# Performance work log

Hardware: AMD Instinct MI355X
Metric: run time of the kernel (lower is better)

## Reference

```python
import jax, jax.numpy as jnp
import numpy as np
import math

B, H, W, Cv, Ct, T = 8, 64, 64, 256, 512, 100
TOP_M = 5
N_PAD = 8  # last N_PAD text tokens are all-zero padding


def _xavier(key, fi, fo):
    lim = math.sqrt(6.0 / (fi + fo))
    return jax.random.uniform(key, (fi, fo), jnp.float32, -lim, lim)


def layernorm(x, g, b, eps=1e-5):
    m = x.mean(-1, keepdims=True)
    v = ((x - m) ** 2).mean(-1, keepdims=True)
    return (x - m) * jax.lax.rsqrt(v + eps) * g + b


def l2norm(x, eps=1e-6):
    n = jnp.sqrt((x * x).sum(-1, keepdims=True))
    return x / jnp.maximum(n, eps)


def setup_inputs() -> dict:
    key = jax.random.key(0)
    ks = jax.random.split(key, 10)
    visual = jax.random.normal(ks[0], (B, H, W, Cv), jnp.float32)
    text = jax.random.normal(ks[1], (B, T, Ct), jnp.float32)
    text = text.at[:, T - N_PAD:, :].set(0.0)  # padded tokens
    return {
        'visual_features': visual,
        'text_features': text,
        'ln1_g': jnp.ones((Cv,), jnp.float32),
        'ln1_b': jnp.zeros((Cv,), jnp.float32),
        'qw': _xavier(ks[2], Cv, Ct), 'qb': jnp.zeros((Ct,), jnp.float32),
        'vw': _xavier(ks[3], Ct, Cv), 'vb': jnp.zeros((Cv,), jnp.float32),
        'gate_w': jax.random.normal(ks[4], (Cv, 1), jnp.float32) * 0.02,
        'gate_b': jnp.zeros((1,), jnp.float32),
        'logit_scale': jnp.asarray(math.log(1.0 / 0.07), jnp.float32),
        'alpha': jnp.asarray(0.1, jnp.float32),
        'ln2_g': jnp.ones((Cv,), jnp.float32),
        'ln2_b': jnp.zeros((Cv,), jnp.float32),
        'w1': jax.random.normal(ks[5], (Cv, 4 * Cv), jnp.float32) * 0.02,
        'b1': jnp.zeros((4 * Cv,), jnp.float32),
        'w2': jax.random.normal(ks[6], (4 * Cv, Cv), jnp.float32) * 0.02,
        'b2': jnp.zeros((Cv,), jnp.float32),
        'top_m': TOP_M,
    }


def reference(visual_features, text_features, ln1_g, ln1_b, qw, qb, vw, vb,
              gate_w, gate_b, logit_scale, alpha, ln2_g, ln2_b, w1, b1, w2, b2,
              top_m):
    Bv, Hh, Ww, C = visual_features.shape
    N = Hh * Ww
    x = layernorm(visual_features, ln1_g, ln1_b).reshape(Bv, N, C)
    q = l2norm(x @ qw + qb)                     # (B,N,Ct)
    k = l2norm(text_features)                   # (B,T,Ct)
    v = text_features @ vw + vb                 # (B,T,Cv)
    pad = jnp.abs(text_features).sum(-1) <= 1e-6  # (B,T) True = padding
    Ctd = float(qw.shape[1])
    scale = jnp.exp(jnp.clip(logit_scale, -2.0, 2.0)) / math.sqrt(Ctd)
    sim = jnp.einsum('bnc,btc->bnt', q, k) * scale
    top_vals, top_idx = jax.lax.top_k(sim, top_m)       # (B,N,M)
    pad_top = jax.vmap(lambda p, i: p[i])(pad, top_idx)  # (B,N,M)
    top_vals = jnp.where(pad_top, -jnp.inf, top_vals)
    attn = jax.nn.softmax(top_vals, axis=-1)
    v_sel = jax.vmap(lambda vb_, ib: vb_[ib])(v, top_idx)  # (B,N,M,Cv)
    aligned = jnp.einsum('bnm,bnmc->bnc', attn, v_sel)
    gate = jax.nn.sigmoid(x @ gate_w + gate_b)  # (B,N,1)
    aligned = aligned * gate
    y = x + alpha * aligned
    y = layernorm(y, ln2_g, ln2_b)
    y = y + (jax.nn.gelu(y @ w1 + b1, approximate=False) @ w2 + b2)
    return y.reshape(Bv, Hh, Ww, C)
```

## Files before the change

kernel.cpp:

```cpp
#include <hip/hip_runtime.h>
#include <hip/hip_bf16.h>
#include <math.h>

using bf16 = __hip_bfloat16;
typedef __attribute__((ext_vector_type(8))) short s16x8;
typedef __attribute__((ext_vector_type(4))) short s16x4;
typedef __attribute__((ext_vector_type(4))) float f32x4;
typedef __attribute__((ext_vector_type(4))) unsigned int u32x4;

static __device__ __forceinline__ float bits2f(unsigned short u) {
  union { unsigned int i; float f; } c; c.i = ((unsigned int)u) << 16; return c.f;
}
static __device__ __forceinline__ unsigned short f2bits(float f) {
  bf16 h = __float2bfloat16(f);
  return *reinterpret_cast<unsigned short*>(&h);
}
static __device__ __forceinline__ unsigned short scrub16(unsigned short u, unsigned short repl) {
  return ((u & 0x7F80u) == 0x7F80u) ? repl : u;
}
static __device__ __forceinline__ unsigned short f2bits_s(float f, unsigned short repl) {
  return scrub16(f2bits(f), repl);
}
static __device__ __forceinline__ float ldf_s(const float* p, float repl) {
  unsigned int w = *reinterpret_cast<const unsigned int*>(p);
  if ((w & 0x7F800000u) == 0x7F800000u) return repl;
  union { unsigned int i; float f; } c; c.i = w; return c.f;
}
static __device__ __forceinline__ float stf_s(float f, float repl) {
  union { float f; unsigned int i; } c; c.f = f;
  if ((c.i & 0x7F800000u) == 0x7F800000u) return repl;
  return f;
}
static __device__ __forceinline__ void gload_lds16(const unsigned short* g, unsigned short* l) {
  __builtin_amdgcn_global_load_lds(
      (const __attribute__((address_space(1))) void*)g,
      (__attribute__((address_space(3))) void*)l, 16, 0, 0);
}

static __device__ __forceinline__ float block_sum(float v, float* red, int tid) {
  #pragma unroll
  for (int o = 32; o > 0; o >>= 1) v += __shfl_down(v, o, 64);
  __syncthreads();
  if ((tid & 63) == 0) red[tid >> 6] = v;
  __syncthreads();
  return red[0] + red[1] + red[2] + red[3];
}

__global__ __launch_bounds__(256)
void k_ln1(float* vis, const float* __restrict__ g, const float* __restrict__ bta) {
  const int lane = threadIdx.x & 63;
  const long row = (long)blockIdx.x * 4 + (threadIdx.x >> 6);
  float* rp = vis + row * 256;
  union { u32x4 u; float f[4]; unsigned int w[4]; } c;
  c.u = *reinterpret_cast<const u32x4*>(&rp[lane * 4]);
  #pragma unroll
  for (int e = 0; e < 4; e++)
    if ((c.w[e] & 0x7F800000u) == 0x7F800000u) c.f[e] = 0.f;
  float s = c.f[0] + c.f[1] + c.f[2] + c.f[3];
  #pragma unroll
  for (int o = 32; o > 0; o >>= 1) s += __shfl_xor(s, o, 64);
  const float mean = s * (1.f / 256.f);
  float vr = 0.f;
  #pragma unroll
  for (int e = 0; e < 4; e++) { c.f[e] -= mean; vr = fmaf(c.f[e], c.f[e], vr); }
  #pragma unroll
  for (int o = 32; o > 0; o >>= 1) vr += __shfl_xor(vr, o, 64);
  const float rstd = rsqrtf(vr * (1.f / 256.f) + 1e-5f);
  f32x4 outv;
  #pragma unroll
  for (int e = 0; e < 4; e++)
    outv[e] = stf_s(c.f[e] * rstd * g[lane * 4 + e] + bta[lane * 4 + e], 0.f);
  *reinterpret_cast<f32x4*>(&rp[lane * 4]) = outv;
}

__global__ __launch_bounds__(256)
void k_prepw(const float* __restrict__ qw, unsigned short* __restrict__ qwt) {
  const int n = blockIdx.x;
  const int k = threadIdx.x;
  qwt[n * 256 + (k ^ ((n & 7) << 3))] = f2bits_s(ldf_s(&qw[(long)k * 512 + n], 0.f), 0);
}

__global__ __launch_bounds__(256)
void k_prep2(const float* __restrict__ text, unsigned short* __restrict__ khat,
             int* __restrict__ padf) {
  __shared__ float red[4];
  const int t = blockIdx.x, b = blockIdx.y, tid = threadIdx.x;
  unsigned short* kr = khat + ((long)b * 112 + t) * 512;
  if (t >= 100) {
    if (tid < 64) *reinterpret_cast<s16x8*>(&kr[tid * 8]) = (s16x8){0,0,0,0,0,0,0,0};
    return;
  }
  const float* tr = text + ((long)b * 100 + t) * 512;
  const float v0 = ldf_s(&tr[tid], 0.f), v1 = ldf_s(&tr[tid + 256], 0.f);
  const float ss = block_sum(fmaf(v0, v0, v1 * v1), red, tid);
  const float sa = block_sum(fabsf(v0) + fabsf(v1), red, tid);
  const float inv = 1.f / fmaxf(sqrtf(ss), 1e-6f);
  kr[tid]       = f2bits_s(v0 * inv, 0);
  kr[tid + 256] = f2bits_s(v1 * inv, 0);
  if (tid == 0) padf[b * 100 + t] = (sa <= 1e-6f) ? 1 : 0;
}

__global__ __launch_bounds__(512)
void k_sim_mfma(const float* __restrict__ x, const unsigned short* __restrict__ qwt,
                const float* __restrict__ qb, const unsigned short* __restrict__ khat,
                const float* __restrict__ ls, unsigned short* __restrict__ simb) {
  __shared__ __align__(16) unsigned short s_q[64][520];
  __shared__ __align__(16) unsigned short s_un[32768];
  __shared__ float s_qn[64];

  const int tid  = threadIdx.x;
  const int lane = tid & 63;
  const int w    = tid >> 6;
  const int l15  = lane & 15;
  const int lg   = lane >> 4;
  const int b    = blockIdx.y;
  const long grow = (long)b * 4096 + (long)blockIdx.x * 64;

  const int R1 = (w >> 2) * 32;
  s16x8 xa[2][8];
  #pragma unroll
  for (int rb = 0; rb < 2; rb++) {
    const float* xr = &x[(grow + R1 + rb * 16 + l15) * 256];
    #pragma unroll
    for (int ks = 0; ks < 8; ks++) {
      const float* p = xr + ks * 32 + lg * 8;
      s16x8 v;
      #pragma unroll
      for (int e = 0; e < 8; e++) v[e] = (short)f2bits_s(ldf_s(p + e, 0.f), 0);
      xa[rb][ks] = v;
    }
  }

  const int C1 = (w & 3) * 32;
  for (int nc = 0; nc < 4; nc++) {
    __syncthreads();
    {
      const unsigned short* src = qwt + (long)nc * 128 * 256;
      #pragma unroll
      for (int it = 0; it < 8; it++) {
        const int u = tid + it * 512;
        *reinterpret_cast<s16x8*>(&s_un[u * 8]) =
            *reinterpret_cast<const s16x8*>(&src[u * 8]);
      }
    }
    __syncthreads();
    f32x4 a1[2][2];
    #pragma unroll
    for (int i = 0; i < 2; i++)
      #pragma unroll
      for (int j = 0; j < 2; j++) a1[i][j] = (f32x4){0.f, 0.f, 0.f, 0.f};
    #pragma unroll
    for (int ks = 0; ks < 8; ks++) {
      s16x8 bfr[2];
      #pragma unroll
      for (int cb = 0; cb < 2; cb++) {
        const int nl = C1 + cb * 16 + l15;
        const int byt = nl * 512 + ((ks * 64 + lg * 16) ^ ((nl & 7) << 4));
        bfr[cb] = *reinterpret_cast<const s16x8*>(reinterpret_cast<const char*>(s_un) + byt);
      }
      #pragma unroll
      for (int rb = 0; rb < 2; rb++) {
        a1[rb][0] = __builtin_amdgcn_mfma_f32_16x16x32_bf16(xa[rb][ks], bfr[0], a1[rb][0], 0, 0, 0);
        a1[rb][1] = __builtin_amdgcn_mfma_f32_16x16x32_bf16(xa[rb][ks], bfr[1], a1[rb][1], 0, 0, 0);
      }
    }
    #pragma unroll
    for (int cb = 0; cb < 2; cb++) {
      const int n = nc * 128 + C1 + cb * 16 + l15;
      const float bq = ldf_s(&qb[n], 0.f);
      #pragma unroll
      for (int rb = 0; rb < 2; rb++)
        #pragma unroll
        for (int rg = 0; rg < 4; rg++)
          s_q[R1 + rb * 16 + lg * 4 + rg][n] = f2bits_s(a1[rb][cb][rg] + bq, 0);
    }
  }
  __syncthreads();

  {
    const int r = tid >> 3, ts8 = tid & 7;
    float ss = 0.f;
    #pragma unroll
    for (int j = 0; j < 8; j++) {
      s16x8 v = *reinterpret_cast<const s16x8*>(&s_q[r][ts8 * 64 + j * 8]);
      #pragma unroll
      for (int e = 0; e < 8; e++) { float f = bits2f((unsigned short)v[e]); ss = fmaf(f, f, ss); }
    }
    #pragma unroll
    for (int o = 4; o > 0; o >>= 1) ss += __shfl_down(ss, o, 8);
    if (ts8 == 0) s_qn[r] = fmaxf(sqrtf(ss), 1e-6f);
  }

  const int wr = w & 1, wc = w >> 1;
  unsigned short (*s_k)[264] = reinterpret_cast<unsigned short(*)[264]>(s_un);
  f32x4 acc[2][2];
  #pragma unroll
  for (int i = 0; i < 2; i++)
    #pragma unroll
    for (int j = 0; j < 2; j++) acc[i][j] = (f32x4){0.f, 0.f, 0.f, 0.f};

  for (int kc = 0; kc < 2; kc++) {
    __syncthreads();
    for (int it = 0; it < 7; it++) {
      const int u = it * 512 + tid;
      const int t = u >> 5, kb = (u & 31) * 8;
      *reinterpret_cast<s16x8*>(&s_k[t][kb]) =
          *reinterpret_cast<const s16x8*>(&khat[((long)b * 112 + t) * 512 + kc * 256 + kb]);
    }
    __syncthreads();
    #pragma unroll
    for (int ks = 0; ks < 8; ks++) {
      const int ko = kc * 256 + ks * 32 + lg * 8;
      s16x8 af[2], bfr[2];
      #pragma unroll
      for (int rb = 0; rb < 2; rb++)
        af[rb] = *reinterpret_cast<const s16x8*>(&s_q[(2 * wr + rb) * 16 + l15][ko]);
      #pragma unroll
      for (int cb = 0; cb < 2; cb++)
        if (2 * wc + cb < 7)
          bfr[cb] = *reinterpret_cast<const s16x8*>(&s_k[(2 * wc + cb) * 16 + l15][ks * 32 + lg * 8]);
      #pragma unroll
      for (int rb = 0; rb < 2; rb++)
        #pragma unroll
        for (int cb = 0; cb < 2; cb++)
          if (2 * wc + cb < 7)
            acc[rb][cb] = __builtin_amdgcn_mfma_f32_16x16x32_bf16(af[rb], bfr[cb], acc[rb][cb], 0, 0, 0);
    }
  }

  float l = ldf_s(&ls[0], 0.f);
  l = fminf(fmaxf(l, -2.f), 2.f);
  const float scale = expf(l) * 0.04419417382415922f;
  #pragma unroll
  for (int rb = 0; rb < 2; rb++)
    #pragma unroll
    for (int rg = 0; rg < 4; rg++) {
      const int row = (2 * wr + rb) * 16 + lg * 4 + rg;
      const float inv = scale / s_qn[row];
      #pragma unroll
      for (int cb = 0; cb < 2; cb++) {
        const int tcol = (2 * wc + cb) * 16 + l15;
        if (2 * wc + cb < 7 && tcol < 100)
          simb[(grow + row) * 100 + tcol] = f2bits_s(acc[rb][cb][rg] * inv, 0);
      }
    }
}

__global__ __launch_bounds__(256)
void k_v(const float* __restrict__ text, const float* __restrict__ vw,
         const float* __restrict__ vb_, float* __restrict__ vf) {
  __shared__ float s_t[512];
  const int bt = blockIdx.x;
  const int tid = threadIdx.x;
  const float* tr = text + (long)bt * 512;
  s_t[tid]       = ldf_s(&tr[tid], 0.f);
  s_t[tid + 256] = ldf_s(&tr[tid + 256], 0.f);
  __syncthreads();
  float acc = 0.f;
  for (int k = 0; k < 512; k++) acc = fmaf(s_t[k], vw[k * 256 + tid], acc);
  vf[(long)bt * 256 + tid] = stf_s(acc + vb_[tid], 0.f);
}

#define AROWS 32
__global__ __launch_bounds__(256)
void k_attn(const unsigned short* __restrict__ sim, const int* __restrict__ pad,
            const float* __restrict__ v, float* xy,
            const float* __restrict__ gate_w, const float* __restrict__ gate_b,
            const float* __restrict__ alpha, const float* __restrict__ ln2g,
            const float* __restrict__ ln2b) {
  __shared__ float s_x[AROWS][256];
  __shared__ float s_sim[AROWS][104];
  __shared__ float s_attn[AROWS][8];
  __shared__ int   s_idx[AROWS][8];
  __shared__ float s_gate[AROWS], s_mu[AROWS], s_rs[AROWS];
  __shared__ int   s_pad[128];
  const int b = blockIdx.y;
  const int n0 = blockIdx.x * AROWS;
  const int tid = threadIdx.x;
  const long xbase = ((long)b * 4096 + n0) * 256;
  #pragma unroll
  for (int i = 0; i < AROWS; i++)
    s_x[i][tid] = ldf_s(&xy[xbase + (long)i * 256 + tid], 0.f);
  const long sbase = ((long)b * 4096 + n0) * 100;
  for (int i = tid; i < AROWS * 100; i += 256) {
    int rr = i / 100, t = i - rr * 100;
    s_sim[rr][t] = bits2f(scrub16(sim[sbase + (long)rr * 100 + t], 0));
  }
  if (tid < 100) s_pad[tid] = pad[b * 100 + tid];
  __syncthreads();

  const int r = tid >> 3, ts = tid & 7;
  float loc[13];
  #pragma unroll
  for (int j = 0; j < 13; j++) {
    int t = ts * 13 + j;
    loc[j] = (t < 100) ? s_sim[r][t] : -1e38f;
  }
  float topv[5]; int topi[5];
  for (int it = 0; it < 5; it++) {
    float bv = -1e38f; int bi = 1 << 20;
    #pragma unroll
    for (int j = 0; j < 13; j++) {
      if (loc[j] > bv) { bv = loc[j]; bi = ts * 13 + j; }
    }
    #pragma unroll
    for (int o = 4; o > 0; o >>= 1) {
      float ov = __shfl_down(bv, o, 8);
      int   oi = __shfl_down(bi, o, 8);
      if (ov > bv || (ov == bv && oi < bi)) { bv = ov; bi = oi; }
    }
    bv = __shfl(bv, 0, 8); bi = __shfl(bi, 0, 8);
    const int bic = (bi < 0) ? 0 : (bi > 99 ? 99 : bi);
    topv[it] = bv; topi[it] = bic;
    const int rel = bi - ts * 13;
    if (rel >= 0 && rel < 13) loc[rel] = -1e38f;
  }
  {
    float tv[5], mx = -1e38f;
    #pragma unroll
    for (int m = 0; m < 5; m++) { tv[m] = s_pad[topi[m]] ? -1e38f : topv[m]; mx = fmaxf(mx, tv[m]); }
    const float mxs = (mx > -1e37f) ? mx : 0.f;
    float se = 0.f, ev[5];
    #pragma unroll
    for (int m = 0; m < 5; m++) {
      ev[m] = (tv[m] > -1e37f) ? expf(fminf(tv[m] - mxs, 0.f)) : 0.f;
      se += ev[m];
    }
    const float rse = (se > 0.f) ? 1.f / se : 0.f;
    if (ts == 0) {
      #pragma unroll
      for (int m = 0; m < 5; m++) { s_attn[r][m] = ev[m] * rse; s_idx[r][m] = topi[m]; }
    }
  }
  {
    float gd = 0.f;
    #pragma unroll
    for (int j = 0; j < 32; j++) {
      int c = ts + 8 * j;
      gd = fmaf(s_x[r][c], gate_w[c], gd);
    }
    #pragma unroll
    for (int o = 4; o > 0; o >>= 1) gd += __shfl_down(gd, o, 8);
    if (ts == 0) s_gate[r] = 1.f / (1.f + expf(fminf(-(gd + gate_b[0]), 80.f)));
  }
  __syncthreads();
  const float al = alpha[0];
  const float* vb_ = v + (long)b * 100 * 256;
  for (int rr = 0; rr < AROWS; rr++) {
    float acc = 0.f;
    #pragma unroll
    for (int m = 0; m < 5; m++)
      acc = fmaf(s_attn[rr][m], ldf_s(&vb_[(long)s_idx[rr][m] * 256 + tid], 0.f), acc);
    s_x[rr][tid] = s_x[rr][tid] + al * (acc * s_gate[rr]);
  }
  __syncthreads();
  {
    float sm = 0.f;
    #pragma unroll
    for (int j = 0; j < 32; j++) sm += s_x[r][ts + 8 * j];
    #pragma unroll
    for (int o = 4; o > 0; o >>= 1) sm += __shfl_down(sm, o, 8);
    sm = __shfl(sm, 0, 8);
    const float mean = sm * (1.f / 256.f);
    float vr = 0.f;
    #pragma unroll
    for (int j = 0; j < 32; j++) { float d = s_x[r][ts + 8 * j] - mean; vr = fmaf(d, d, vr); }
    #pragma unroll
    for (int o = 4; o > 0; o >>= 1) vr += __shfl_down(vr, o, 8);
    if (ts == 0) { s_mu[r] = mean; s_rs[r] = rsqrtf(vr * (1.f / 256.f) + 1e-5f); }
  }
  __syncthreads();
  for (int rr = 0; rr < AROWS; rr++) {
    float yv = (s_x[rr][tid] - s_mu[rr]) * s_rs[rr] * ln2g[tid] + ln2b[tid];
    xy[xbase + (long)rr * 256 + tid] = stf_s(yv, 100.0f);
  }
}

__global__ __launch_bounds__(256)
void k_prep(const float* __restrict__ w1, const float* __restrict__ w2,
            unsigned short* __restrict__ w1s, unsigned short* __restrict__ w2s) {
  const int i = blockIdx.x * 256 + threadIdx.x;
  if (i < 262144) {
    const int h = i >> 8, k = i & 255;
    w1s[h * 256 + (k ^ ((h & 7) << 3))] = f2bits(w1[(long)k * 1024 + h]);
  } else {
    const int j = i - 262144;
    const int c = j >> 10, h = j & 1023;
    const int hs = (h & ~63) | ((h & 63) ^ ((c & 7) << 3));
    w2s[(long)c * 1024 + hs] = f2bits(w2[(long)h * 256 + c]);
  }
}

__global__ __launch_bounds__(512, 2)
void k_ffn_mfma(const float* __restrict__ yln,
                const unsigned short* __restrict__ w1s,
                const float* __restrict__ b1,
                const unsigned short* __restrict__ w2s,
                const float* __restrict__ b2,
                float* __restrict__ out) {
  __shared__ __align__(16) unsigned short s_w1[64 * 256];
  __shared__ __align__(16) unsigned short s_w2[256 * 64];
  __shared__ __align__(16) unsigned short s_h[128][72];

  const int tid  = threadIdx.x;
  const int lane = tid & 63;
  const int w    = tid >> 6;
  const int l15  = lane & 15;
  const int lg   = lane >> 4;
  const long gr0 = (long)blockIdx.x * 128;

  #pragma unroll
  for (int it = 0; it < 4; it++) {
    const int u = tid + it * 512;
    gload_lds16(&w1s[u * 8], &s_w1[u * 8]);
  }

  const int R1 = (w >> 1) * 32, C1 = (w & 1) * 32;
  const int R0 = (w >> 2) * 64, C0 = (w & 3) * 64;

  s16x8 ya[2][8];
  #pragma unroll
  for (int rb = 0; rb < 2; rb++) {
    const float* xr = &yln[(gr0 + R1 + rb * 16 + l15) * 256];
    #pragma unroll
    for (int ks = 0; ks < 8; ks++) {
      const float* p = xr + ks * 32 + lg * 8;
      s16x8 v;
      #pragma unroll
      for (int e = 0; e < 8; e++) v[e] = (short)f2bits_s(ldf_s(p + e, 0.f), 0);
      ya[rb][ks] = v;
    }
  }

  f32x4 acc[4][4];
  #pragma unroll
  for (int i = 0; i < 4; i++)
    #pragma unroll
    for (int j = 0; j < 4; j++)
      acc[i][j] = (f32x4){0.f, 0.f, 0.f, 0.f};

  __syncthreads();

  for (int kc = 0; kc < 16; kc++) {
    const int hc = kc * 64;
    #pragma unroll
    for (int it = 0; it < 4; it++) {
      const int u = tid + it * 512;
      const int c = u >> 3, k8 = (u & 7) * 8;
      gload_lds16(&w2s[(long)c * 1024 + hc + k8], &s_w2[u * 8]);
    }

    f32x4 a1[2][2];
    #pragma unroll
    for (int i = 0; i < 2; i++)
      #pragma unroll
      for (int j = 0; j < 2; j++) a1[i][j] = (f32x4){0.f, 0.f, 0.f, 0.f};
    __builtin_amdgcn_s_setprio(1);
    #pragma unroll
    for (int ks = 0; ks < 8; ks++) {
      const int ko = ks * 32 + lg * 8;
      const int n0_ = C1 + l15, n1_ = C1 + 16 + l15;
      const s16x8 bf0 = *reinterpret_cast<const s16x8*>(&s_w1[n0_ * 256 + (ko ^ ((n0_ & 7) << 3))]);
      const s16x8 bf1 = *reinterpret_cast<const s16x8*>(&s_w1[n1_ * 256 + (ko ^ ((n1_ & 7) << 3))]);
      a1[0][0] = __builtin_amdgcn_mfma_f32_16x16x32_bf16(ya[0][ks], bf0, a1[0][0], 0, 0, 0);
      a1[0][1] = __builtin_amdgcn_mfma_f32_16x16x32_bf16(ya[0][ks], bf1, a1[0][1], 0, 0, 0);
      a1[1][0] = __builtin_amdgcn_mfma_f32_16x16x32_bf16(ya[1][ks], bf0, a1[1][0], 0, 0, 0);
      a1[1][1] = __builtin_amdgcn_mfma_f32_16x16x32_bf16(ya[1][ks], bf1, a1[1][1], 0, 0, 0);
    }
    __builtin_amdgcn_s_setprio(0);
    #pragma unroll
    for (int cb = 0; cb < 2; cb++) {
      const int col = C1 + cb * 16 + l15;
      const float bb = b1[hc + col];
      #pragma unroll
      for (int rb = 0; rb < 2; rb++)
        #pragma unroll
        for (int rg = 0; rg < 4; rg++) {
          const float t = a1[rb][cb][rg] + bb;
          const float g = 0.5f * t * (1.f + erff(t * 0.7071067811865475f));
          s_h[R1 + rb * 16 + lg * 4 + rg][col] = f2bits_s(g, 0);
        }
    }
    __syncthreads();

    if (kc < 15) {
      #pragma unroll
      for (int it = 0; it < 4; it++) {
        const int u = tid + it * 512;
        gload_lds16(&w1s[(long)(hc + 64) * 256 + u * 8], &s_w1[u * 8]);
      }
    }

    __builtin_amdgcn_s_setprio(1);
    #pragma unroll
    for (int p = 0; p < 2; p++) {
      const int ko = p * 32 + lg * 8;
      s16x8 bfr[4];
      #pragma unroll
      for (int cb = 0; cb < 4; cb++) {
        const int c = C0 + cb * 16 + l15;
        bfr[cb] = *reinterpret_cast<const s16x8*>(&s_w2[c * 64 + (ko ^ ((c & 7) << 3))]);
      }
      #pragma unroll
      for (int rb = 0; rb < 4; rb++) {
        const s16x8 af = *reinterpret_cast<const s16x8*>(&s_h[R0 + rb * 16 + l15][ko]);
        #pragma unroll
        for (int cb = 0; cb < 4; cb++)
          acc[rb][cb] = __builtin_amdgcn_mfma_f32_16x16x32_bf16(af, bfr[cb], acc[rb][cb], 0, 0, 0);
      }
    }
    __builtin_amdgcn_s_setprio(0);
    __syncthreads();
  }

  #pragma unroll
  for (int rb = 0; rb < 4; rb++)
    #pragma unroll
    for (int rg = 0; rg < 4; rg++) {
      const int R = R0 + rb * 16 + lg * 4 + rg;
      const float* yr = &yln[(gr0 + R) * 256];
      #pragma unroll
      for (int cb = 0; cb < 4; cb++) {
        const int C = C0 + cb * 16 + l15;
        out[(gr0 + R) * 256 + C] =
            stf_s(ldf_s(&yr[C], 0.f) + acc[rb][cb][rg] + b2[C], 300.0f);
      }
    }
}

#define FR 32
__global__ __launch_bounds__(256)
void k_ffn(const float* __restrict__ yln, const float* __restrict__ w1,
           const float* __restrict__ b1, const float* __restrict__ w2,
           const float* __restrict__ b2, float* __restrict__ out) {
  __shared__ unsigned short s_y[FR][256];
  __shared__ float s_h[FR][66];
  __shared__ unsigned short s_w[64 * 256];
  const int tid = threadIdx.x;
  const long gr0 = (long)blockIdx.x * FR;
  for (int i = tid; i < FR * 256; i += 256)
    (&s_y[0][0])[i] = f2bits_s(ldf_s(&yln[gr0 * 256 + i], 0.f), 0);
  const int ty = tid >> 4, tx = tid & 15;
  const int r = tid >> 3, ts = tid & 7;
  float acc[32];
  #pragma unroll
  for (int j = 0; j < 32; j++) acc[j] = 0.f;
  for (int kc = 0; kc < 16; kc++) {
    __syncthreads();
    for (int i = tid; i < 64 * 256; i += 256) {
      int kk = i >> 6, c = i & 63;
      s_w[i] = f2bits(w1[(long)kk * 1024 + kc * 64 + c]);
    }
    __syncthreads();
    {
      float a2[2][4] = {{0.f,0.f,0.f,0.f},{0.f,0.f,0.f,0.f}};
      for (int k = 0; k < 256; k++) {
        const float a0 = bits2f(s_y[ty * 2][k]);
        const float a1 = bits2f(s_y[ty * 2 + 1][k]);
        #pragma unroll
        for (int j = 0; j < 4; j++) {
          const float bv = bits2f(s_w[k * 64 + tx * 4 + j]);
          a2[0][j] = fmaf(a0, bv, a2[0][j]);
          a2[1][j] = fmaf(a1, bv, a2[1][j]);
        }
      }
      #pragma unroll
      for (int i = 0; i < 2; i++)
        #pragma unroll
        for (int j = 0; j < 4; j++) {
          float t = a2[i][j] + b1[kc * 64 + tx * 4 + j];
          s_h[ty * 2 + i][tx * 4 + j] = 0.5f * t * (1.f + erff(t * 0.7071067811865475f));
        }
    }
    __syncthreads();
    for (int i = tid; i < 64 * 256; i += 256) {
      int kk = i >> 8, c = i & 255;
      s_w[i] = f2bits(w2[(long)(kc * 64 + kk) * 256 + c]);
    }
    __syncthreads();
    for (int kk = 0; kk < 64; kk++) {
      const float hv = s_h[r][kk];
      #pragma unroll
      for (int jj = 0; jj < 8; jj++) {
        #pragma unroll
        for (int u = 0; u < 4; u++) {
          const float wv = bits2f(s_w[kk * 256 + ts * 4 + 32 * jj + u]);
          acc[jj * 4 + u] = fmaf(hv, wv, acc[jj * 4 + u]);
        }
      }
    }
  }
  #pragma unroll
  for (int jj = 0; jj < 8; jj++) {
    #pragma unroll
    for (int u = 0; u < 4; u++) {
      int c = ts * 4 + 32 * jj + u;
      out[(gr0 + r) * 256 + c] = stf_s(bits2f(s_y[r][c]) + acc[jj * 4 + u] + b2[c], 300.0f);
    }
  }
}

__global__ __launch_bounds__(256)
void k_fill(float* __restrict__ out, long n, float V) {
  long i = (long)blockIdx.x * 256 + threadIdx.x;
  if (i < n) out[i] = V;
}

extern "C" void kernel_launch(void* const* d_in, const int* in_sizes, int n_in,
                              void* d_out, int out_size, void* d_ws, size_t ws_size,
                              hipStream_t stream) {
  static const int DEXP[19] = {8388608,409600,256,256,131072,512,131072,256,256,1,
                               1,1,256,256,262144,1024,262144,256,1};
  static const int S19[19] = {15,12,6,5,11,10,16,14,4,3,9,0,8,7,17,1,18,2,13};
  static const int S18[18] = {14,12,6,5,11,10,15,13,4,3,9,0,8,7,16,1,17,2};
  static const int ID19[19] = {0,1,2,3,4,5,6,7,8,9,10,11,12,13,14,15,16,17,18};

  auto okmap = [&](const int* P, int cnt, int need_n) -> bool {
    if (n_in != need_n) return false;
    for (int i = 0; i < cnt; i++)
      if (in_sizes[P[i]] != DEXP[i]) return false;
    return true;
  };

  const int* M = nullptr;
  if      (okmap(S19, 19, 19)) M = S19;
  else if (okmap(S18, 18, 18)) M = S18;
  else if (okmap(ID19, 19, 19) || okmap(ID19, 18, 18)) M = ID19;

  if (!M) {
    float V;
    if (n_in == 19 || n_in == 18) {
      int bad = 0;
      while (bad < n_in && bad < 19 && in_sizes[bad] == DEXP[bad]) bad++;
      V = 1024.f * (float)(1 + bad);
    } else {
      V = 32.f * (float)n_in + 16.f;
    }
    long n = (long)out_size;
    k_fill<<<(int)((n + 255) / 256), 256, 0, stream>>>((float*)d_out, n, V);
    return;
  }

  float*       vis  = (float*)d_in[M[0]];
  const float* text = (const float*)d_in[M[1]];
  const float* ln1g = (const float*)d_in[M[2]];
  const float* ln1b = (const float*)d_in[M[3]];
  const float* qw   = (const float*)d_in[M[4]];
  const float* qb   = (const float*)d_in[M[5]];
  const float* vw   = (const float*)d_in[M[6]];
  const float* vb   = (const float*)d_in[M[7]];
  const float* gw   = (const float*)d_in[M[8]];
  const float* gb   = (const float*)d_in[M[9]];
  const float* ls   = (const float*)d_in[M[10]];
  const float* alp  = (const float*)d_in[M[11]];
  const float* ln2g = (const float*)d_in[M[12]];
  const float* ln2b = (const float*)d_in[M[13]];
  const float* w1   = (const float*)d_in[M[14]];
  const float* b1   = (const float*)d_in[M[15]];
  const float* w2   = (const float*)d_in[M[16]];
  const float* b2   = (const float*)d_in[M[17]];

  unsigned short* simb = (unsigned short*)d_out;
  float* vf   = (float*)((char*)d_out + 6553600);
  int*   padf = (int*)  ((char*)d_out + 7372800);
  unsigned short* qwt  = (unsigned short*)((char*)d_out + 7376000);
  unsigned short* khat = (unsigned short*)((char*)d_out + 7900288);
  float* outp = (float*)d_out;

  const bool mfma_ffn = (d_ws != nullptr) && (ws_size >= (size_t)1048576);
  unsigned short* w1s = (unsigned short*)d_ws;
  unsigned short* w2s = w1s + 262144;

  k_ln1 <<<8192, 256, 0, stream>>>(vis, ln1g, ln1b);
  if (mfma_ffn)
    k_prep<<<2048, 256, 0, stream>>>(w1, w2, w1s, w2s);
  k_prepw<<<512, 256, 0, stream>>>(qw, qwt);
  k_prep2<<<dim3(112, 8), 256, 0, stream>>>(text, khat, padf);
  k_sim_mfma<<<dim3(64, 8), 512, 0, stream>>>(vis, qwt, qb, khat, ls, simb);
  k_v   <<<800, 256, 0, stream>>>(text, vw, vb, vf);
  k_attn<<<dim3(128, 8), 256, 0, stream>>>(simb, padf, vf, vis, gw, gb, alp, ln2g, ln2b);
  if (mfma_ffn)
    k_ffn_mfma<<<256, 512, 0, stream>>>(vis, w1s, b1, w2s, b2, outp);
  else
    k_ffn <<<1024, 256, 0, stream>>>(vis, w1, b1, w2, b2, outp);
}
```

Baseline: 294.5 us.

## Use direct global-to-LDS loads, vectorized fp32 packing and tanh-form GELU

Weight tiles for the query projection and the key tiles in the similarity kernel are now loaded with global_load_lds instead of register round-trips. The khat layout is pre-swizzled in prep so the padded LDS array is no longer needed. Activation rows are read as float4 pairs before bf16 packing in both the sim and MLP kernels. The exact erf GELU is replaced by a tanh-style approximation using exp and fast divide. This reduces load instructions and transcendental cost, but changes GELU numerics slightly.

```diff
diff --git a/kernel.cpp b/kernel.cpp
--- a/kernel.cpp
+++ b/kernel.cpp
@@ -30,6 +30,25 @@
   union { float f; unsigned int i; } c; c.f = f;
   if ((c.i & 0x7F800000u) == 0x7F800000u) return repl;
   return f;
+}
+static __device__ __forceinline__ s16x8 pack8(const float* p) {
+  union { f32x4 f; float fe[4]; unsigned int u[4]; } a, b;
+  a.f = *reinterpret_cast<const f32x4*>(p);
+  b.f = *reinterpret_cast<const f32x4*>(p + 4);
+  s16x8 v;
+  #pragma unroll
+  for (int e = 0; e < 4; e++) {
+    const float fa = ((a.u[e] & 0x7F800000u) == 0x7F800000u) ? 0.f : a.fe[e];
+    const float fb = ((b.u[e] & 0x7F800000u) == 0x7F800000u) ? 0.f : b.fe[e];
+    v[e]     = (short)f2bits_s(fa, 0);
+    v[e + 4] = (short)f2bits_s(fb, 0);
+  }
+  return v;
+}
+static __device__ __forceinline__ float gelu_fast(float t) {
+  const float u = fmaf(0.044715f * t * t, t, t);
+  const float e = __expf(-1.5957691216057308f * u);
+  return __fdividef(t, 1.f + e);
 }
 static __device__ __forceinline__ void gload_lds16(const unsigned short* g, unsigned short* l) {
   __builtin_amdgcn_global_load_lds(
@@ -95,8 +114,9 @@
   const float ss = block_sum(fmaf(v0, v0, v1 * v1), red, tid);
   const float sa = block_sum(fabsf(v0) + fabsf(v1), red, tid);
   const float inv = 1.f / fmaxf(sqrtf(ss), 1e-6f);
-  kr[tid]       = f2bits_s(v0 * inv, 0);
-  kr[tid + 256] = f2bits_s(v1 * inv, 0);
+  const int ks = tid ^ ((t & 7) << 3);
+  kr[ks]       = f2bits_s(v0 * inv, 0);
+  kr[ks + 256] = f2bits_s(v1 * inv, 0);
   if (tid == 0) padf[b * 100 + t] = (sa <= 1e-6f) ? 1 : 0;
 }
 
@@ -116,34 +136,25 @@
   const int b    = blockIdx.y;
   const long grow = (long)b * 4096 + (long)blockIdx.x * 64;
 
+  #pragma unroll
+  for (int it = 0; it < 8; it++) {
+    const int u = tid + it * 512;
+    gload_lds16(&qwt[u * 8], &s_un[u * 8]);
+  }
+
   const int R1 = (w >> 2) * 32;
   s16x8 xa[2][8];
   #pragma unroll
   for (int rb = 0; rb < 2; rb++) {
     const float* xr = &x[(grow + R1 + rb * 16 + l15) * 256];
     #pragma unroll
-    for (int ks = 0; ks < 8; ks++) {
-      const float* p = xr + ks * 32 + lg * 8;
-      s16x8 v;
-      #pragma unroll
-      for (int e = 0; e < 8; e++) v[e] = (short)f2bits_s(ldf_s(p + e, 0.f), 0);
-      xa[rb][ks] = v;
-    }
-  }
+    for (int ks = 0; ks < 8; ks++)
+      xa[rb][ks] = pack8(xr + ks * 32 + lg * 8);
+  }
+  __syncthreads();
 
   const int C1 = (w & 3) * 32;
   for (int nc = 0; nc < 4; nc++) {
-    __syncthreads();
-    {
-      const unsigned short* src = qwt + (long)nc * 128 * 256;
-      #pragma unroll
-      for (int it = 0; it < 8; it++) {
-        const int u = tid + it * 512;
-        *reinterpret_cast<s16x8*>(&s_un[u * 8]) =
-            *reinterpret_cast<const s16x8*>(&src[u * 8]);
-      }
-    }
-    __syncthreads();
     f32x4 a1[2][2];
     #pragma unroll
     for (int i = 0; i < 2; i++)
@@ -174,8 +185,17 @@
         for (int rg = 0; rg < 4; rg++)
           s_q[R1 + rb * 16 + lg * 4 + rg][n] = f2bits_s(a1[rb][cb][rg] + bq, 0);
     }
-  }
-  __syncthreads();
+    __syncthreads();
+    if (nc < 3) {
+      const unsigned short* src = qwt + (long)(nc + 1) * 32768;
+      #pragma unroll
+      for (int it = 0; it < 8; it++) {
+        const int u = tid + it * 512;
+        gload_lds16(&src[u * 8], &s_un[u * 8]);
+      }
+      __syncthreads();
+    }
+  }
 
   {
     const int r = tid >> 3, ts8 = tid & 7;
@@ -192,7 +212,6 @@
   }
 
   const int wr = w & 1, wc = w >> 1;
-  unsigned short (*s_k)[264] = reinterpret_cast<unsigned short(*)[264]>(s_un);
   f32x4 acc[2][2];
   #pragma unroll
   for (int i = 0; i < 2; i++)
@@ -200,12 +219,11 @@
     for (int j = 0; j < 2; j++) acc[i][j] = (f32x4){0.f, 0.f, 0.f, 0.f};
 
   for (int kc = 0; kc < 2; kc++) {
-    __syncthreads();
+    #pragma unroll
     for (int it = 0; it < 7; it++) {
       const int u = it * 512 + tid;
       const int t = u >> 5, kb = (u & 31) * 8;
-      *reinterpret_cast<s16x8*>(&s_k[t][kb]) =
-          *reinterpret_cast<const s16x8*>(&khat[((long)b * 112 + t) * 512 + kc * 256 + kb]);
+      gload_lds16(&khat[((long)b * 112 + t) * 512 + kc * 256 + kb], &s_un[u * 8]);
     }
     __syncthreads();
     #pragma unroll
@@ -217,8 +235,11 @@
         af[rb] = *reinterpret_cast<const s16x8*>(&s_q[(2 * wr + rb) * 16 + l15][ko]);
       #pragma unroll
       for (int cb = 0; cb < 2; cb++)
-        if (2 * wc + cb < 7)
-          bfr[cb] = *reinterpret_cast<const s16x8*>(&s_k[(2 * wc + cb) * 16 + l15][ks * 32 + lg * 8]);
+        if (2 * wc + cb < 7) {
+          const int t = (2 * wc + cb) * 16 + l15;
+          bfr[cb] = *reinterpret_cast<const s16x8*>(
+              &s_un[t * 256 + ((ks * 32 + lg * 8) ^ ((t & 7) << 3))]);
+        }
       #pragma unroll
       for (int rb = 0; rb < 2; rb++)
         #pragma unroll
@@ -226,6 +247,7 @@
           if (2 * wc + cb < 7)
             acc[rb][cb] = __builtin_amdgcn_mfma_f32_16x16x32_bf16(af[rb], bfr[cb], acc[rb][cb], 0, 0, 0);
     }
+    __syncthreads();
   }
 
   float l = ldf_s(&ls[0], 0.f);
@@ -423,13 +445,8 @@
   for (int rb = 0; rb < 2; rb++) {
     const float* xr = &yln[(gr0 + R1 + rb * 16 + l15) * 256];
     #pragma unroll
-    for (int ks = 0; ks < 8; ks++) {
-      const float* p = xr + ks * 32 + lg * 8;
-      s16x8 v;
-      #pragma unroll
-      for (int e = 0; e < 8; e++) v[e] = (short)f2bits_s(ldf_s(p + e, 0.f), 0);
-      ya[rb][ks] = v;
-    }
+    for (int ks = 0; ks < 8; ks++)
+      ya[rb][ks] = pack8(xr + ks * 32 + lg * 8);
   }
 
   f32x4 acc[4][4];
@@ -477,8 +494,7 @@
         #pragma unroll
         for (int rg = 0; rg < 4; rg++) {
           const float t = a1[rb][cb][rg] + bb;
-          const float g = 0.5f * t * (1.f + erff(t * 0.7071067811865475f));
-          s_h[R1 + rb * 16 + lg * 4 + rg][col] = f2bits_s(g, 0);
+          s_h[R1 + rb * 16 + lg * 4 + rg][col] = f2bits_s(gelu_fast(t), 0);
         }
     }
     __syncthreads();
```

After: 294.9 us. No clear change (+0.1%).
